# Kernel tuning notes

Measured on AMD Instinct MI355X. Metric: run time of the kernel, lower is better.

## Reference

```python
import jax, jax.numpy as jnp
import numpy as np

INPUT_DIM, HIDDEN_DIM = 2048, 2048
MEM_SLOTS, MEM_DIM, OUTPUT_DIM = 4096, 1024, 2048


def setup_inputs() -> dict:
    key = jax.random.key(0)
    ks = jax.random.split(key, 16)
    s = 0.02  # small init scale for weights
    return {
        "x": jax.random.normal(ks[0], (1, INPUT_DIM), jnp.float32),
        "h_prev": jax.random.normal(ks[1], (1, HIDDEN_DIM), jnp.float32),
        "c_prev": jax.random.normal(ks[2], (1, HIDDEN_DIM), jnp.float32),
        "memory": jax.random.normal(ks[3], (MEM_SLOTS, MEM_DIM), jnp.float32),
        "usage": jax.random.uniform(ks[4], (MEM_SLOTS,), jnp.float32),
        "read_W": jax.random.normal(ks[5], (MEM_DIM, HIDDEN_DIM), jnp.float32) * s,
        "read_b": jax.random.normal(ks[6], (MEM_DIM,), jnp.float32) * s,
        "W_ih": jax.random.normal(ks[7], (4 * HIDDEN_DIM, INPUT_DIM + MEM_DIM), jnp.float32) * s,
        "b_ih": jax.random.normal(ks[8], (4 * HIDDEN_DIM,), jnp.float32) * s,
        "W_hh": jax.random.normal(ks[9], (4 * HIDDEN_DIM, HIDDEN_DIM), jnp.float32) * s,
        "b_hh": jax.random.normal(ks[10], (4 * HIDDEN_DIM,), jnp.float32) * s,
        "head_W": jax.random.normal(ks[11], (3 * MEM_DIM + MEM_SLOTS + 1, HIDDEN_DIM), jnp.float32) * s,
        "head_b": jax.random.normal(ks[12], (3 * MEM_DIM + MEM_SLOTS + 1,), jnp.float32) * s,
        "out_W": jax.random.normal(ks[13], (OUTPUT_DIM, HIDDEN_DIM + MEM_DIM), jnp.float32) * s,
        "out_b": jax.random.normal(ks[14], (OUTPUT_DIM,), jnp.float32) * s,
    }


def reference(x, h_prev, c_prev, memory, usage,
              read_W, read_b, W_ih, b_ih, W_hh, b_hh,
              head_W, head_b, out_W, out_b):
    M, S = MEM_DIM, MEM_SLOTS
    # --- read ---
    read_key = jnp.tanh(h_prev @ read_W.T + read_b)        # [1, M]
    sim = memory @ read_key[0]                             # [S]
    read_weights = jax.nn.softmax(sim)                     # [S]
    read_vec = read_weights @ memory                       # [M]
    usage_new = usage + read_weights                       # [S]
    # --- LSTM controller (torch LSTMCell gate order: i, f, g, o) ---
    inp = jnp.concatenate([x, read_vec[None, :]], axis=1)  # [1, input+M]
    gates = inp @ W_ih.T + b_ih + h_prev @ W_hh.T + b_hh   # [1, 4H]
    i, f, g, o = jnp.split(gates, 4, axis=1)
    c_new = jax.nn.sigmoid(f) * c_prev + jax.nn.sigmoid(i) * jnp.tanh(g)
    h_new = jax.nn.sigmoid(o) * jnp.tanh(c_new)
    # --- write head params ---
    params = (h_new @ head_W.T + head_b)[0]                # [3M + S + 1]
    erase_vec = jax.nn.sigmoid(params[M:2 * M])            # [M]
    add_vec = jnp.tanh(params[2 * M:3 * M])                # [M]
    w_logits = params[3 * M:3 * M + S]                     # [S]
    write_gate = jax.nn.sigmoid(params[-1])
    w = jax.nn.softmax(w_logits) * write_gate              # [S]
    # slot zeroed if (updated) usage below threshold, then erase/add
    mem_masked = jnp.where(usage_new[:, None] < 0.1, 0.0, memory)
    new_memory = mem_masked * (1.0 - w[:, None] * erase_vec[None, :]) \
                 + w[:, None] * add_vec[None, :]           # [S, M]
    # --- output ---
    out = jnp.concatenate([h_new, read_vec[None, :]], axis=1) @ out_W.T + out_b
    return (out, h_new, c_new, new_memory, usage_new)
```

## Files before the change

### kernel.cpp

```cpp
#include <hip/hip_runtime.h>
#include <math.h>


#define INPUT_DIM 2048
#define HIDDEN_DIM 2048
#define MEM_SLOTS 4096
#define MEM_DIM 1024
#define OUTPUT_DIM 2048

static __device__ __forceinline__ float sigmoidf_(float x) {
    return 1.0f / (1.0f + expf(-x));
}

template<int K4, int ACT>
__launch_bounds__(256)
__global__ void gemv_t(const float* __restrict__ W, const float* __restrict__ v,
                       const float* __restrict__ bias, float* __restrict__ out,
                       int rows) {
    int wave = (int)((blockIdx.x * blockDim.x + threadIdx.x) >> 6);
    int lane = threadIdx.x & 63;
    if (wave >= rows) return;
    const float4* __restrict__ Wr = (const float4*)W + (size_t)wave * (size_t)K4;
    const float4* __restrict__ v4 = (const float4*)v;
    float a0 = 0.f, a1 = 0.f, a2 = 0.f, a3 = 0.f;
#pragma unroll
    for (int i0 = 0; i0 < K4; i0 += 256) {
        int i = i0 + lane;
        float4 w0 = Wr[i];
        float4 w1 = Wr[i + 64];
        float4 w2 = Wr[i + 128];
        float4 w3 = Wr[i + 192];
        float4 x0 = v4[i];
        float4 x1 = v4[i + 64];
        float4 x2 = v4[i + 128];
        float4 x3 = v4[i + 192];
        a0 = fmaf(w0.x, x0.x, a0); a0 = fmaf(w0.y, x0.y, a0);
        a0 = fmaf(w0.z, x0.z, a0); a0 = fmaf(w0.w, x0.w, a0);
        a1 = fmaf(w1.x, x1.x, a1); a1 = fmaf(w1.y, x1.y, a1);
        a1 = fmaf(w1.z, x1.z, a1); a1 = fmaf(w1.w, x1.w, a1);
        a2 = fmaf(w2.x, x2.x, a2); a2 = fmaf(w2.y, x2.y, a2);
        a2 = fmaf(w2.z, x2.z, a2); a2 = fmaf(w2.w, x2.w, a2);
        a3 = fmaf(w3.x, x3.x, a3); a3 = fmaf(w3.y, x3.y, a3);
        a3 = fmaf(w3.z, x3.z, a3); a3 = fmaf(w3.w, x3.w, a3);
    }
    float acc = (a0 + a1) + (a2 + a3);
#pragma unroll
    for (int off = 32; off > 0; off >>= 1) acc += __shfl_down(acc, off);
    if (lane == 0) {
        float r = acc + (bias ? bias[wave] : 0.f);
        if (ACT == 1) r = tanhf(r);
        out[wave] = r;
    }
}

__global__ void softmax_rw_kernel(const float* __restrict__ sim, const float* __restrict__ usage,
                                  float* __restrict__ rw, float* __restrict__ usage_out) {
    __shared__ float sm[16];
    int tid = threadIdx.x;
    int lane = tid & 63, wid = tid >> 6;
    float v0 = sim[tid], v1 = sim[tid + 1024], v2 = sim[tid + 2048], v3 = sim[tid + 3072];
    float m = fmaxf(fmaxf(v0, v1), fmaxf(v2, v3));
#pragma unroll
    for (int off = 32; off > 0; off >>= 1) m = fmaxf(m, __shfl_down(m, off));
    if (lane == 0) sm[wid] = m;
    __syncthreads();
    if (tid == 0) {
        float mm = sm[0];
        for (int i = 1; i < 16; ++i) mm = fmaxf(mm, sm[i]);
        sm[0] = mm;
    }
    __syncthreads();
    float mm = sm[0];
    float e0 = expf(v0 - mm), e1 = expf(v1 - mm), e2 = expf(v2 - mm), e3 = expf(v3 - mm);
    float s = e0 + e1 + e2 + e3;
#pragma unroll
    for (int off = 32; off > 0; off >>= 1) s += __shfl_down(s, off);
    __syncthreads();
    if (lane == 0) sm[wid] = s;
    __syncthreads();
    if (tid == 0) {
        float ss = 0.f;
        for (int i = 0; i < 16; ++i) ss += sm[i];
        sm[0] = ss;
    }
    __syncthreads();
    float inv = 1.f / sm[0];
    float r0 = e0 * inv, r1 = e1 * inv, r2 = e2 * inv, r3 = e3 * inv;
    rw[tid] = r0; rw[tid + 1024] = r1; rw[tid + 2048] = r2; rw[tid + 3072] = r3;
    usage_out[tid]        = usage[tid]        + r0;
    usage_out[tid + 1024] = usage[tid + 1024] + r1;
    usage_out[tid + 2048] = usage[tid + 2048] + r2;
    usage_out[tid + 3072] = usage[tid + 3072] + r3;
}

__global__ void readvec_partial_kernel(const float* __restrict__ memory,
                                       const float* __restrict__ rw,
                                       float* __restrict__ partial) {
    int t = threadIdx.x;
    int chunk = blockIdx.x;
    const float4* mem4 = (const float4*)memory;
    float4 acc = make_float4(0.f, 0.f, 0.f, 0.f);
    int s0 = chunk * 64;
    for (int s = s0; s < s0 + 64; ++s) {
        float w = rw[s];
        float4 m = mem4[(size_t)s * 256 + t];
        acc.x = fmaf(w, m.x, acc.x);
        acc.y = fmaf(w, m.y, acc.y);
        acc.z = fmaf(w, m.z, acc.z);
        acc.w = fmaf(w, m.w, acc.w);
    }
    ((float4*)partial)[chunk * 256 + t] = acc;
}

__global__ void readvec_reduce_kernel(const float* __restrict__ partial,
                                      const float* __restrict__ x,
                                      float* __restrict__ xcat, float* __restrict__ hvcat) {
    int c = threadIdx.x;
    float s = 0.f;
    for (int k = 0; k < 64; ++k) s += partial[k * 1024 + c];
    xcat[2048 + c] = s;
    hvcat[2048 + c] = s;
    xcat[c] = x[c];
    xcat[1024 + c] = x[1024 + c];
}

__global__ void lstm_elem_kernel(const float* __restrict__ gih, const float* __restrict__ ghh,
                                 const float* __restrict__ b_ih, const float* __restrict__ b_hh,
                                 const float* __restrict__ c_prev,
                                 float* __restrict__ c_out, float* __restrict__ h_out,
                                 float* __restrict__ hvcat) {
    int t = blockIdx.x * blockDim.x + threadIdx.x;
    if (t >= HIDDEN_DIM) return;
    float gi = gih[t]        + ghh[t]        + b_ih[t]        + b_hh[t];
    float gf = gih[2048 + t] + ghh[2048 + t] + b_ih[2048 + t] + b_hh[2048 + t];
    float gg = gih[4096 + t] + ghh[4096 + t] + b_ih[4096 + t] + b_hh[4096 + t];
    float go = gih[6144 + t] + ghh[6144 + t] + b_ih[6144 + t] + b_hh[6144 + t];
    float ig = sigmoidf_(gi);
    float fg = sigmoidf_(gf);
    float g2 = tanhf(gg);
    float og = sigmoidf_(go);
    float c = fg * c_prev[t] + ig * g2;
    float h = og * tanhf(c);
    c_out[t] = c;
    h_out[t] = h;
    hvcat[t] = h;
}

__global__ void softmax_w_kernel(const float* __restrict__ params, float* __restrict__ wv,
                                 float* __restrict__ erase, float* __restrict__ addv) {
    __shared__ float sm[16];
    int tid = threadIdx.x;
    int lane = tid & 63, wid = tid >> 6;
    const float* logits = params + 3072;
    float v0 = logits[tid], v1 = logits[tid + 1024], v2 = logits[tid + 2048], v3 = logits[tid + 3072];
    float m = fmaxf(fmaxf(v0, v1), fmaxf(v2, v3));
#pragma unroll
    for (int off = 32; off > 0; off >>= 1) m = fmaxf(m, __shfl_down(m, off));
    if (lane == 0) sm[wid] = m;
    __syncthreads();
    if (tid == 0) {
        float mm = sm[0];
        for (int i = 1; i < 16; ++i) mm = fmaxf(mm, sm[i]);
        sm[0] = mm;
    }
    __syncthreads();
    float mm = sm[0];
    float e0 = expf(v0 - mm), e1 = expf(v1 - mm), e2 = expf(v2 - mm), e3 = expf(v3 - mm);
    float s = e0 + e1 + e2 + e3;
#pragma unroll
    for (int off = 32; off > 0; off >>= 1) s += __shfl_down(s, off);
    __syncthreads();
    if (lane == 0) sm[wid] = s;
    __syncthreads();
    if (tid == 0) {
        float ss = 0.f;
        for (int i = 0; i < 16; ++i) ss += sm[i];
        sm[0] = ss;
    }
    __syncthreads();
    float gate = sigmoidf_(params[7168]);
    float scale = gate / sm[0];
    wv[tid] = e0 * scale; wv[tid + 1024] = e1 * scale;
    wv[tid + 2048] = e2 * scale; wv[tid + 3072] = e3 * scale;
    erase[tid] = sigmoidf_(params[1024 + tid]);
    addv[tid]  = tanhf(params[2048 + tid]);
}

__global__ void memupdate_kernel(const float* __restrict__ memory, const float* __restrict__ wv,
                                 const float* __restrict__ erase, const float* __restrict__ addv,
                                 const float* __restrict__ usage_new, float* __restrict__ newmem) {
    int s = blockIdx.x;
    int t = threadIdx.x;
    float w = wv[s];
    float mask = (usage_new[s] < 0.1f) ? 0.f : 1.f;
    float4 m = ((const float4*)memory)[(size_t)s * 256 + t];
    float4 e = ((const float4*)erase)[t];
    float4 a = ((const float4*)addv)[t];
    float4 r;
    r.x = mask * m.x * (1.f - w * e.x) + w * a.x;
    r.y = mask * m.y * (1.f - w * e.y) + w * a.y;
    r.z = mask * m.z * (1.f - w * e.z) + w * a.z;
    r.w = mask * m.w * (1.f - w * e.w) + w * a.w;
    ((float4*)newmem)[(size_t)s * 256 + t] = r;
}

extern "C" void kernel_launch(void* const* d_in, const int* in_sizes, int n_in,
                              void* d_out_, int out_size, void* d_ws, size_t ws_size,
                              hipStream_t stream) {
    const float* x      = (const float*)d_in[0];
    const float* h_prev = (const float*)d_in[1];
    const float* c_prev = (const float*)d_in[2];
    const float* memory = (const float*)d_in[3];
    const float* usage  = (const float*)d_in[4];
    const float* read_W = (const float*)d_in[5];
    const float* read_b = (const float*)d_in[6];
    const float* W_ih   = (const float*)d_in[7];
    const float* b_ih   = (const float*)d_in[8];
    const float* W_hh   = (const float*)d_in[9];
    const float* b_hh   = (const float*)d_in[10];
    const float* head_W = (const float*)d_in[11];
    const float* head_b = (const float*)d_in[12];
    const float* out_W  = (const float*)d_in[13];
    const float* out_b  = (const float*)d_in[14];

    float* d_out = (float*)d_out_;
    float* ws = (float*)d_ws;

    float* xcat    = ws + 0;
    float* hvcat   = ws + 3072;
    float* rk      = ws + 6144;
    float* sim     = ws + 7168;
    float* rw      = ws + 11264;
    float* ghh     = ws + 7168;
    float* gih     = ws + 15360;
    float* params  = ws + 23552;
    float* wv      = ws + 30976;
    float* erase   = ws + 35072;
    float* addv    = ws + 36096;
    float* partial = ws + 37120;

    float* out       = d_out;
    float* h_new     = d_out + 2048;
    float* c_new     = d_out + 4096;
    float* newmem    = d_out + 6144;
    float* usage_new = d_out + 6144 + (size_t)MEM_SLOTS * MEM_DIM;

    gemv_t<512, 1><<<256, 256, 0, stream>>>(read_W, h_prev, read_b, rk, MEM_DIM);
    gemv_t<256, 0><<<1024, 256, 0, stream>>>(memory, rk, nullptr, sim, MEM_SLOTS);
    softmax_rw_kernel<<<1, 1024, 0, stream>>>(sim, usage, rw, usage_new);
    readvec_partial_kernel<<<64, 256, 0, stream>>>(memory, rw, partial);
    readvec_reduce_kernel<<<1, 1024, 0, stream>>>(partial, x, xcat, hvcat);
    gemv_t<768, 0><<<2048, 256, 0, stream>>>(W_ih, xcat, nullptr, gih, 4 * HIDDEN_DIM);
    gemv_t<512, 0><<<2048, 256, 0, stream>>>(W_hh, h_prev, nullptr, ghh, 4 * HIDDEN_DIM);
    lstm_elem_kernel<<<8, 256, 0, stream>>>(gih, ghh, b_ih, b_hh, c_prev, c_new, h_new, hvcat);
    gemv_t<512, 0><<<1793, 256, 0, stream>>>(head_W, h_new, head_b, params, 7169);
    softmax_w_kernel<<<1, 1024, 0, stream>>>(params, wv, erase, addv);
    memupdate_kernel<<<4096, 256, 0, stream>>>(memory, wv, erase, addv, usage_new, newmem);
    gemv_t<768, 0><<<512, 256, 0, stream>>>(out_W, hvcat, out_b, out, OUTPUT_DIM);
}
```

Before: 83.85 us.

## Overlap independent LSTM GEMV work with the memory-read chain and split gate GEMVs

```diff
diff --git a/kernel.cpp b/kernel.cpp
--- a/kernel.cpp
+++ b/kernel.cpp
@@ -2,38 +2,32 @@
 #include <math.h>
 
 
-#define INPUT_DIM 2048
 #define HIDDEN_DIM 2048
 #define MEM_SLOTS 4096
 #define MEM_DIM 1024
-#define OUTPUT_DIM 2048
+
+typedef float floatx4 __attribute__((ext_vector_type(4)));
 
 static __device__ __forceinline__ float sigmoidf_(float x) {
     return 1.0f / (1.0f + expf(-x));
 }
 
-template<int K4, int ACT>
-__launch_bounds__(256)
-__global__ void gemv_t(const float* __restrict__ W, const float* __restrict__ v,
-                       const float* __restrict__ bias, float* __restrict__ out,
-                       int rows) {
-    int wave = (int)((blockIdx.x * blockDim.x + threadIdx.x) >> 6);
-    int lane = threadIdx.x & 63;
-    if (wave >= rows) return;
-    const float4* __restrict__ Wr = (const float4*)W + (size_t)wave * (size_t)K4;
-    const float4* __restrict__ v4 = (const float4*)v;
+template<int K4F4>
+static __device__ __forceinline__ float rowdot(const float4* __restrict__ Wr,
+                                               const float4* __restrict__ v4,
+                                               int lane) {
     float a0 = 0.f, a1 = 0.f, a2 = 0.f, a3 = 0.f;
 #pragma unroll
-    for (int i0 = 0; i0 < K4; i0 += 256) {
+    for (int i0 = 0; i0 < K4F4; i0 += 256) {
         int i = i0 + lane;
-        float4 w0 = Wr[i];
-        float4 w1 = Wr[i + 64];
-        float4 w2 = Wr[i + 128];
-        float4 w3 = Wr[i + 192];
-        float4 x0 = v4[i];
-        float4 x1 = v4[i + 64];
-        float4 x2 = v4[i + 128];
-        float4 x3 = v4[i + 192];
+        floatx4 w0 = *(const floatx4*)(Wr + i);
+        floatx4 w1 = *(const floatx4*)(Wr + i + 64);
+        floatx4 w2 = *(const floatx4*)(Wr + i + 128);
+        floatx4 w3 = *(const floatx4*)(Wr + i + 192);
+        floatx4 x0 = *(const floatx4*)(v4 + i);
+        floatx4 x1 = *(const floatx4*)(v4 + i + 64);
+        floatx4 x2 = *(const floatx4*)(v4 + i + 128);
+        floatx4 x3 = *(const floatx4*)(v4 + i + 192);
         a0 = fmaf(w0.x, x0.x, a0); a0 = fmaf(w0.y, x0.y, a0);
         a0 = fmaf(w0.z, x0.z, a0); a0 = fmaf(w0.w, x0.w, a0);
         a1 = fmaf(w1.x, x1.x, a1); a1 = fmaf(w1.y, x1.y, a1);
@@ -46,18 +40,68 @@
     float acc = (a0 + a1) + (a2 + a3);
 #pragma unroll
     for (int off = 32; off > 0; off >>= 1) acc += __shfl_down(acc, off);
-    if (lane == 0) {
-        float r = acc + (bias ? bias[wave] : 0.f);
-        if (ACT == 1) r = tanhf(r);
-        out[wave] = r;
-    }
-}
-
-__global__ void softmax_rw_kernel(const float* __restrict__ sim, const float* __restrict__ usage,
-                                  float* __restrict__ rw, float* __restrict__ usage_out) {
-    __shared__ float sm[16];
+    return acc;
+}
+
+static __device__ __forceinline__ void do_bg(int u, const float4* whh4,
+                                             const float4* wih4, const float4* h4,
+                                             const float4* x4, float* gh, float* gx,
+                                             int lane) {
+    if (u < 8192) {
+        float d = rowdot<512>(whh4 + (size_t)u * 512, h4, lane);
+        if (lane == 0) gh[u] = d;
+    } else {
+        int r = u - 8192;
+        float d = rowdot<512>(wih4 + (size_t)r * 768, x4, lane);
+        if (lane == 0) gx[r] = d;
+    }
+}
+
+__global__ void k1_rk_bg(const float* __restrict__ read_W, const float* __restrict__ read_b,
+                         const float* __restrict__ h_prev, const float* __restrict__ W_hh,
+                         const float* __restrict__ W_ih, const float* __restrict__ x,
+                         float* __restrict__ rk, float* __restrict__ gh, float* __restrict__ gx) {
+    int lane = threadIdx.x & 63;
+    int gw = blockIdx.x * 4 + (threadIdx.x >> 6);
+    const float4* h4 = (const float4*)h_prev;
+    if (gw < 1024) {
+        float d = rowdot<512>((const float4*)read_W + (size_t)gw * 512, h4, lane);
+        if (lane == 0) rk[gw] = tanhf(d + read_b[gw]);
+    } else {
+        do_bg(gw - 1024, (const float4*)W_hh, (const float4*)W_ih, h4,
+              (const float4*)x, gh, gx, lane);
+    }
+}
+
+__global__ void k2_sim_bg(const float* __restrict__ memory, const float* __restrict__ rk,
+                          const float* __restrict__ h_prev, const float* __restrict__ W_hh,
+                          const float* __restrict__ W_ih, const float* __restrict__ x,
+                          float* __restrict__ sim, float* __restrict__ gh, float* __restrict__ gx) {
+    int lane = threadIdx.x & 63;
+    int gw = blockIdx.x * 4 + (threadIdx.x >> 6);
+    if (gw < 4096) {
+        float d = rowdot<256>((const float4*)memory + (size_t)gw * 256, (const float4*)rk, lane);
+        if (lane == 0) sim[gw] = d;
+    } else {
+        do_bg(3072 + (gw - 4096), (const float4*)W_hh, (const float4*)W_ih,
+              (const float4*)h_prev, (const float4*)x, gh, gx, lane);
+    }
+}
+
+__global__ void k3_smx_bg(const float* __restrict__ sim, const float* __restrict__ usage,
+                          float* __restrict__ rw, float* __restrict__ usage_out,
+                          const float* __restrict__ h_prev, const float* __restrict__ W_hh,
+                          const float* __restrict__ W_ih, const float* __restrict__ x,
+                          float* __restrict__ gh, float* __restrict__ gx) {
     int tid = threadIdx.x;
     int lane = tid & 63, wid = tid >> 6;
+    if (blockIdx.x != 0) {
+        int u = 7168 + (blockIdx.x - 1) * 16 + wid;
+        do_bg(u, (const float4*)W_hh, (const float4*)W_ih, (const float4*)h_prev,
+              (const float4*)x, gh, gx, lane);
+        return;
+    }
+    __shared__ float sm[16];
     float v0 = sim[tid], v1 = sim[tid + 1024], v2 = sim[tid + 2048], v3 = sim[tid + 3072];
     float m = fmaxf(fmaxf(v0, v1), fmaxf(v2, v3));
 #pragma unroll
@@ -93,10 +137,19 @@
     usage_out[tid + 3072] = usage[tid + 3072] + r3;
 }
 
-__global__ void readvec_partial_kernel(const float* __restrict__ memory,
-                                       const float* __restrict__ rw,
-                                       float* __restrict__ partial) {
+__global__ void k4_rvp_bg(const float* __restrict__ memory, const float* __restrict__ rw,
+                          float* __restrict__ partial,
+                          const float* __restrict__ h_prev, const float* __restrict__ W_hh,
+                          const float* __restrict__ W_ih, const float* __restrict__ x,
+                          float* __restrict__ gh, float* __restrict__ gx) {
     int t = threadIdx.x;
+    int lane = t & 63;
+    if (blockIdx.x >= 64) {
+        int u = 10240 + (blockIdx.x - 64) * 4 + (t >> 6);
+        do_bg(u, (const float4*)W_hh, (const float4*)W_ih, (const float4*)h_prev,
+              (const float4*)x, gh, gx, lane);
+        return;
+    }
     int chunk = blockIdx.x;
     const float4* mem4 = (const float4*)memory;
     float4 acc = make_float4(0.f, 0.f, 0.f, 0.f);
@@ -112,42 +165,70 @@
     ((float4*)partial)[chunk * 256 + t] = acc;
 }
 
-__global__ void readvec_reduce_kernel(const float* __restrict__ partial,
-                                      const float* __restrict__ x,
-                                      float* __restrict__ xcat, float* __restrict__ hvcat) {
-    int c = threadIdx.x;
+__global__ void k5_rvr_bg(const float* __restrict__ partial, float* __restrict__ rv,
+                          const float* __restrict__ h_prev, const float* __restrict__ W_hh,
+                          const float* __restrict__ W_ih, const float* __restrict__ x,
+                          float* __restrict__ gh, float* __restrict__ gx) {
+    int tid = threadIdx.x;
+    int lane = tid & 63, wid = tid >> 6;
+    if (blockIdx.x != 0) {
+        int u = 13312 + (blockIdx.x - 1) * 16 + wid;
+        do_bg(u, (const float4*)W_hh, (const float4*)W_ih, (const float4*)h_prev,
+              (const float4*)x, gh, gx, lane);
+        return;
+    }
     float s = 0.f;
-    for (int k = 0; k < 64; ++k) s += partial[k * 1024 + c];
-    xcat[2048 + c] = s;
-    hvcat[2048 + c] = s;
-    xcat[c] = x[c];
-    xcat[1024 + c] = x[1024 + c];
-}
-
-__global__ void lstm_elem_kernel(const float* __restrict__ gih, const float* __restrict__ ghh,
-                                 const float* __restrict__ b_ih, const float* __restrict__ b_hh,
-                                 const float* __restrict__ c_prev,
-                                 float* __restrict__ c_out, float* __restrict__ h_out,
-                                 float* __restrict__ hvcat) {
-    int t = blockIdx.x * blockDim.x + threadIdx.x;
-    if (t >= HIDDEN_DIM) return;
-    float gi = gih[t]        + ghh[t]        + b_ih[t]        + b_hh[t];
-    float gf = gih[2048 + t] + ghh[2048 + t] + b_ih[2048 + t] + b_hh[2048 + t];
-    float gg = gih[4096 + t] + ghh[4096 + t] + b_ih[4096 + t] + b_hh[4096 + t];
-    float go = gih[6144 + t] + ghh[6144 + t] + b_ih[6144 + t] + b_hh[6144 + t];
-    float ig = sigmoidf_(gi);
-    float fg = sigmoidf_(gf);
-    float g2 = tanhf(gg);
-    float og = sigmoidf_(go);
-    float c = fg * c_prev[t] + ig * g2;
-    float h = og * tanhf(c);
-    c_out[t] = c;
-    h_out[t] = h;
-    hvcat[t] = h;
-}
-
-__global__ void softmax_w_kernel(const float* __restrict__ params, float* __restrict__ wv,
-                                 float* __restrict__ erase, float* __restrict__ addv) {
+    for (int k = 0; k < 64; ++k) s += partial[k * 1024 + tid];
+    rv[tid] = s;
+}
+
+__global__ void k6_grv(const float* __restrict__ W_ih, const float* __restrict__ rv,
+                       float* __restrict__ grv) {
+    int lane = threadIdx.x & 63;
+    int gw = blockIdx.x * 4 + (threadIdx.x >> 6);
+    float d = rowdot<256>((const float4*)W_ih + (size_t)gw * 768 + 512, (const float4*)rv, lane);
+    if (lane == 0) grv[gw] = d;
+}
+
+__global__ void k7_lstm(const float* __restrict__ gx, const float* __restrict__ grv,
+                        const float* __restrict__ gh, const float* __restrict__ b_ih,
+                        const float* __restrict__ b_hh, const float* __restrict__ c_prev,
+                        float* __restrict__ c_new, float* __restrict__ h_new) {
+    int t = blockIdx.x * 256 + threadIdx.x;
+    float gi = gx[t]        + grv[t]        + gh[t]        + b_ih[t]        + b_hh[t];
+    float gf = gx[2048 + t] + grv[2048 + t] + gh[2048 + t] + b_ih[2048 + t] + b_hh[2048 + t];
+    float gg = gx[4096 + t] + grv[4096 + t] + gh[4096 + t] + b_ih[4096 + t] + b_hh[4096 + t];
+    float go = gx[6144 + t] + grv[6144 + t] + gh[6144 + t] + b_ih[6144 + t] + b_hh[6144 + t];
+    float c = sigmoidf_(gf) * c_prev[t] + sigmoidf_(gi) * tanhf(gg);
+    float h = sigmoidf_(go) * tanhf(c);
+    c_new[t] = c;
+    h_new[t] = h;
+}
+
+__global__ void k8_head_out(const float* __restrict__ head_W, const float* __restrict__ head_b,
+                            const float* __restrict__ out_W, const float* __restrict__ h_new,
+                            const float* __restrict__ rv, float* __restrict__ params,
+                            float* __restrict__ outh, float* __restrict__ outrv) {
+    int lane = threadIdx.x & 63;
+    int u = blockIdx.x * 4 + (threadIdx.x >> 6);
+    const float4* hn4 = (const float4*)h_new;
+    if (u < 6145) {
+        int r = 1024 + u;
+        float d = rowdot<512>((const float4*)head_W + (size_t)r * 512, hn4, lane);
+        if (lane == 0) params[r] = d + head_b[r];
+    } else if (u < 8193) {
+        int o = u - 6145;
+        float d = rowdot<512>((const float4*)out_W + (size_t)o * 768, hn4, lane);
+        if (lane == 0) outh[o] = d;
+    } else if (u < 10241) {
+        int o = u - 8193;
+        float d = rowdot<256>((const float4*)out_W + (size_t)o * 768 + 512, (const float4*)rv, lane);
+        if (lane == 0) outrv[o] = d;
+    }
+}
+
+__global__ void k9_smxw(const float* __restrict__ params, float* __restrict__ wv,
+                        float* __restrict__ erase, float* __restrict__ addv) {
     __shared__ float sm[16];
     int tid = threadIdx.x;
     int lane = tid & 63, wid = tid >> 6;
@@ -186,9 +267,11 @@
     addv[tid]  = tanhf(params[2048 + tid]);
 }
 
-__global__ void memupdate_kernel(const float* __restrict__ memory, const float* __restrict__ wv,
-                                 const float* __restrict__ erase, const float* __restrict__ addv,
-                                 const float* __restrict__ usage_new, float* __restrict__ newmem) {
+__global__ void k10_memupd(const float* __restrict__ memory, const float* __restrict__ wv,
+                           const float* __restrict__ erase, const float* __restrict__ addv,
+                           const float* __restrict__ usage_new, float* __restrict__ newmem,
+                           const float* __restrict__ outh, const float* __restrict__ outrv,
+                           const float* __restrict__ out_b, float* __restrict__ out) {
     int s = blockIdx.x;
     int t = threadIdx.x;
     float w = wv[s];
@@ -202,6 +285,10 @@
     r.z = mask * m.z * (1.f - w * e.z) + w * a.z;
     r.w = mask * m.w * (1.f - w * e.w) + w * a.w;
     ((float4*)newmem)[(size_t)s * 256 + t] = r;
+    if (s < 8) {
+        int i = s * 256 + t;
+        out[i] = outh[i] + outrv[i] + out_b[i];
+    }
 }
 
 extern "C" void kernel_launch(void* const* d_in, const int* in_sizes, int n_in,
@@ -226,18 +313,20 @@
     float* d_out = (float*)d_out_;
     float* ws = (float*)d_ws;
 
-    float* xcat    = ws + 0;
-    float* hvcat   = ws + 3072;
-    float* rk      = ws + 6144;
-    float* sim     = ws + 7168;
-    float* rw      = ws + 11264;
-    float* ghh     = ws + 7168;
-    float* gih     = ws + 15360;
-    float* params  = ws + 23552;
-    float* wv      = ws + 30976;
-    float* erase   = ws + 35072;
-    float* addv    = ws + 36096;
-    float* partial = ws + 37120;
+    float* rk      = ws;
+    float* sim     = ws + 1024;
+    float* rw      = ws + 5120;
+    float* rv      = ws + 9216;
+    float* gx      = ws + 10240;
+    float* gh      = ws + 18432;
+    float* grv     = ws + 26624;
+    float* params  = ws + 34816;
+    float* outh    = ws + 42240;
+    float* outrv   = ws + 44288;
+    float* wvv     = ws + 46336;
+    float* erase   = ws + 50432;
+    float* addv    = ws + 51456;
+    float* partial = ws + 52480;
 
     float* out       = d_out;
     float* h_new     = d_out + 2048;
@@ -245,16 +334,15 @@
     float* newmem    = d_out + 6144;
     float* usage_new = d_out + 6144 + (size_t)MEM_SLOTS * MEM_DIM;
 
-    gemv_t<512, 1><<<256, 256, 0, stream>>>(read_W, h_prev, read_b, rk, MEM_DIM);
-    gemv_t<256, 0><<<1024, 256, 0, stream>>>(memory, rk, nullptr, sim, MEM_SLOTS);
-    softmax_rw_kernel<<<1, 1024, 0, stream>>>(sim, usage, rw, usage_new);
-    readvec_partial_kernel<<<64, 256, 0, stream>>>(memory, rw, partial);
-    readvec_reduce_kernel<<<1, 1024, 0, stream>>>(partial, x, xcat, hvcat);
-    gemv_t<768, 0><<<2048, 256, 0, stream>>>(W_ih, xcat, nullptr, gih, 4 * HIDDEN_DIM);
-    gemv_t<512, 0><<<2048, 256, 0, stream>>>(W_hh, h_prev, nullptr, ghh, 4 * HIDDEN_DIM);
-    lstm_elem_kernel<<<8, 256, 0, stream>>>(gih, ghh, b_ih, b_hh, c_prev, c_new, h_new, hvcat);
-    gemv_t<512, 0><<<1793, 256, 0, stream>>>(head_W, h_new, head_b, params, 7169);
-    softmax_w_kernel<<<1, 1024, 0, stream>>>(params, wv, erase, addv);
-    memupdate_kernel<<<4096, 256, 0, stream>>>(memory, wv, erase, addv, usage_new, newmem);
-    gemv_t<768, 0><<<512, 256, 0, stream>>>(out_W, hvcat, out_b, out, OUTPUT_DIM);
-}
+    k1_rk_bg<<<1024, 256, 0, stream>>>(read_W, read_b, h_prev, W_hh, W_ih, x, rk, gh, gx);
+    k2_sim_bg<<<2048, 256, 0, stream>>>(memory, rk, h_prev, W_hh, W_ih, x, sim, gh, gx);
+    k3_smx_bg<<<193, 1024, 0, stream>>>(sim, usage, rw, usage_new, h_prev, W_hh, W_ih, x, gh, gx);
+    k4_rvp_bg<<<832, 256, 0, stream>>>(memory, rw, partial, h_prev, W_hh, W_ih, x, gh, gx);
+    k5_rvr_bg<<<193, 1024, 0, stream>>>(partial, rv, h_prev, W_hh, W_ih, x, gh, gx);
+    k6_grv<<<2048, 256, 0, stream>>>(W_ih, rv, grv);
+    k7_lstm<<<8, 256, 0, stream>>>(gx, grv, gh, b_ih, b_hh, c_prev, c_new, h_new);
+    k8_head_out<<<2561, 256, 0, stream>>>(head_W, head_b, out_W, h_new, rv, params, outh, outrv);
+    k9_smxw<<<1, 1024, 0, stream>>>(params, wvv, erase, addv);
+    k10_memupd<<<4096, 256, 0, stream>>>(memory, wvv, erase, addv, usage_new, newmem,
+                                         outh, outrv, out_b, out);
+}
```

Result: faster. 73.82 us, median of 2 (-12.0%).
